# Optimization experiments

Measured on AMD Instinct MI355X. Metric: run time of the kernel, lower is better.

The kernel has to match this reference:

```python
import jax, jax.numpy as jnp
import numpy as np

NEAR, FAR = 0.05, 6.0
STEPSIZE = 0.5
ALPHA_INIT = 1e-6
XYZ_MIN = np.array([-1.0, -1.0, -1.0], np.float32)
XYZ_MAX = np.array([1.0, 1.0, 1.0], np.float32)
WORLD = (160, 160, 160)
VOXEL_SIZE = 2.0 / 160.0  # ((prod span)/num_voxels)^(1/3)
N_SAMPLES = int(np.linalg.norm(np.array(WORLD) + 1) / STEPSIZE) + 1  # 558
ACT_SHIFT = float(np.log(1.0 / (1.0 - ALPHA_INIT) - 1.0))


def setup_inputs() -> dict:
    key = jax.random.key(0)
    k1, k2, k3, k4, k5, k6, k7 = jax.random.split(key, 7)
    rays_o = (jax.random.uniform(k1, (8192, 3), jnp.float32) - 0.5) * 1.2  # inside bbox
    rd = jax.random.normal(k2, (8192, 3), jnp.float32)
    rays_d = rd / jnp.linalg.norm(rd, axis=-1, keepdims=True)
    jitter = jax.random.uniform(k3, (8192, 1), jnp.float32)
    em_modes = jax.random.randint(k4, (8192,), 0, 2, jnp.int32)
    density = jax.random.normal(k5, (1, 160, 160, 160), jnp.float32) * 0.1
    off_color = jax.random.normal(k6, (3, 160, 160, 160), jnp.float32) * 0.1
    emo_color = jax.random.normal(k7, (3, 160, 160, 160), jnp.float32) * 0.1
    return {"rays_o": rays_o, "rays_d": rays_d, "jitter": jitter, "em_modes": em_modes,
            "density": density, "off_color": off_color, "emo_color": emo_color}


def grid_sampler(pts, grid):
    """Trilinear interp, align_corners=True, zero padding. grid [C,Nx,Ny,Nz], pts [...,3] -> [...,C]."""
    C = grid.shape[0]
    sizes = np.array(grid.shape[1:], np.int32)
    lead = pts.shape[:-1]
    t = (pts.reshape(-1, 3) - XYZ_MIN) / (XYZ_MAX - XYZ_MIN)
    idx = t * (jnp.asarray(sizes, pts.dtype) - 1)  # voxel-space coords
    i0 = jnp.floor(idx).astype(jnp.int32)
    f = idx - i0.astype(pts.dtype)
    out = jnp.zeros((i0.shape[0], C), grid.dtype)
    for corner in range(8):
        off = np.array([(corner >> 2) & 1, (corner >> 1) & 1, corner & 1], np.int32)
        ci = i0 + off  # [N,3]
        w = jnp.prod(jnp.where(off[None, :] == 1, f, 1.0 - f), axis=-1)  # [N]
        valid = jnp.all((ci >= 0) & (ci < sizes[None, :]), axis=-1)
        cc = jnp.clip(ci, 0, sizes[None, :] - 1)
        vals = grid[:, cc[:, 0], cc[:, 1], cc[:, 2]].T  # [N,C]
        out = out + (w * valid)[:, None] * vals
    return out.reshape(*lead, C)


def sample_ray(rays_o, rays_d, jitter):
    vec = jnp.where(rays_d == 0, 1e-6, rays_d)
    rate_a = (XYZ_MAX - rays_o) / vec
    rate_b = (XYZ_MIN - rays_o) / vec
    t_min = jnp.clip(jnp.minimum(rate_a, rate_b).max(-1), NEAR, FAR)
    t_max = jnp.clip(jnp.maximum(rate_a, rate_b).min(-1), NEAR, FAR)
    mask_out = t_max <= t_min  # [R]
    rng = jnp.arange(N_SAMPLES, dtype=rays_o.dtype)[None, :] + jitter  # [R,S]
    step = STEPSIZE * VOXEL_SIZE * rng
    interpx = t_min[:, None] + step / jnp.linalg.norm(rays_d, axis=-1, keepdims=True)
    rays_pts = rays_o[:, None, :] + rays_d[:, None, :] * interpx[..., None]  # [R,S,3]
    mask_out = mask_out[:, None] | ((rays_pts < XYZ_MIN) | (rays_pts > XYZ_MAX)).any(-1)
    return rays_pts, mask_out


def reference(rays_o, rays_d, jitter, em_modes, density, off_color, emo_color):
    rays_pts, mask_out = sample_ray(rays_o, rays_d, jitter)
    dens = grid_sampler(rays_pts, density)[..., 0]  # [R,S]
    alpha_all = 1.0 - jnp.exp(-jax.nn.softplus(dens + ACT_SHIFT) * STEPSIZE)
    alpha = jnp.where(mask_out, 0.0, alpha_all)
    p = jnp.clip(1.0 - alpha, 1e-10, None)
    alphainv_cum = jnp.concatenate([jnp.ones_like(p[..., :1]), jnp.cumprod(p, -1)], -1)  # [R,S+1]
    weights = alpha * alphainv_cum[..., :-1]
    on_mask = (em_modes == 1)[:, None, None]
    emo = jax.nn.sigmoid(grid_sampler(rays_pts, emo_color))
    off = jax.nn.sigmoid(grid_sampler(rays_pts, off_color))
    rgb = jnp.where(on_mask, emo, 0.0) + off  # [R,S,3]
    rgb_marched = (weights[..., None] * rgb).sum(-2)  # [R,3]
    return (alphainv_cum, weights, alphainv_cum[..., -1:], rgb, rgb_marched)
```

## Files before the change

### kernel.cpp

```cpp
#include <hip/hip_runtime.h>
#include <math.h>


namespace {
constexpr int   kR   = 8192;
constexpr int   kS   = 558;
constexpr int   kNC  = (kS + 63) / 64;
constexpr int   kG   = 160;
constexpr int   kG3  = kG * kG * kG;
constexpr float kNear = 0.05f;
constexpr float kFar  = 6.0f;
constexpr float kStepWorld = 0.5f * (2.0f / 160.0f);
constexpr float kActShift = -13.815509557963774f;
constexpr float kLog2e = 1.4426950408889634f;
constexpr int   kBX = 80, kBY = 80, kBZ = 40;
constexpr int   kNB = kBX * kBY * kBZ;
constexpr int   kGridWords = kNB * 16;
constexpr int   kXS = kBY * kBZ * 16;
constexpr int   kYS = kBZ * 16;
}

typedef unsigned int nuint4 __attribute__((ext_vector_type(4)));
typedef float        nfloat2 __attribute__((ext_vector_type(2)));
typedef float        nfloat4 __attribute__((ext_vector_type(4)));

__device__ __forceinline__ float fexp(float x) {
  return __builtin_amdgcn_exp2f(x * kLog2e);
}
__device__ __forceinline__ float sigmoidf_(float x) {
  return __builtin_amdgcn_rcpf(1.0f + fexp(-x));
}

__global__ __launch_bounds__(256) void repack_grids(
    const float* __restrict__ density,
    const float* __restrict__ off_c,
    const float* __restrict__ emo_c,
    unsigned* __restrict__ gridA,
    unsigned* __restrict__ gridB)
{
  const int t   = blockIdx.x * blockDim.x + threadIdx.x;
  const int bid = t >> 2;
  const int q   = t & 3;
  if (bid >= kNB) return;
  const int bz = bid % kBZ;
  const int u  = bid / kBZ;
  const int by = u % kBY;
  const int bx = u / kBY;
  const int x  = bx * 2 + (q >> 1);
  const int y  = by * 2 + (q & 1);
  const int z0 = bz * 4;
  const int vbase = (x * kG + y) * kG + z0;

  const nfloat4 d  = __builtin_nontemporal_load((const nfloat4*)(density + vbase));
  const nfloat4 f0 = __builtin_nontemporal_load((const nfloat4*)(off_c + vbase));
  const nfloat4 f1 = __builtin_nontemporal_load((const nfloat4*)(off_c + vbase + kG3));
  const nfloat4 f2 = __builtin_nontemporal_load((const nfloat4*)(off_c + vbase + 2 * kG3));
  const nfloat4 e0 = __builtin_nontemporal_load((const nfloat4*)(emo_c + vbase));
  const nfloat4 e1 = __builtin_nontemporal_load((const nfloat4*)(emo_c + vbase + kG3));
  const nfloat4 e2 = __builtin_nontemporal_load((const nfloat4*)(emo_c + vbase + 2 * kG3));

  nuint4 va, vb;
  #pragma unroll
  for (int lz = 0; lz < 4; ++lz) {
    int qa = __builtin_amdgcn_cvt_pk_fp8_f32(d[lz],  f0[lz], 0,  false);
    qa     = __builtin_amdgcn_cvt_pk_fp8_f32(f1[lz], f2[lz], qa, true);
    int qb = __builtin_amdgcn_cvt_pk_fp8_f32(e0[lz], e1[lz], 0,  false);
    qb     = __builtin_amdgcn_cvt_pk_fp8_f32(e2[lz], 0.0f,   qb, true);
    va[lz] = (unsigned)qa;
    vb[lz] = (unsigned)qb;
  }
  const size_t woff = (size_t)bid * 16 + q * 4;
  __builtin_nontemporal_store(va, (nuint4*)(gridA + woff));
  __builtin_nontemporal_store(vb, (nuint4*)(gridB + woff));
}

__global__ __launch_bounds__(256) void dvgo_fwd(
    const float* __restrict__ rays_o,
    const float* __restrict__ rays_d,
    const float* __restrict__ jitter,
    const int*   __restrict__ em_modes,
    const unsigned* __restrict__ gridA,
    const unsigned* __restrict__ gridB,
    float* __restrict__ out)
{
  const int tid  = blockIdx.x * blockDim.x + threadIdx.x;
  const int ray  = tid >> 6;
  const int lane = tid & 63;
  if (ray >= kR) return;

  const float ox = rays_o[ray * 3 + 0];
  const float oy = rays_o[ray * 3 + 1];
  const float oz = rays_o[ray * 3 + 2];
  const float dx = rays_d[ray * 3 + 0];
  const float dy = rays_d[ray * 3 + 1];
  const float dz = rays_d[ray * 3 + 2];
  const float jit = jitter[ray];
  const bool  on  = (em_modes[ray] == 1);

  const float vx = (dx == 0.0f) ? 1e-6f : dx;
  const float vy = (dy == 0.0f) ? 1e-6f : dy;
  const float vz = (dz == 0.0f) ? 1e-6f : dz;
  const float ivx = __builtin_amdgcn_rcpf(vx);
  const float ivy = __builtin_amdgcn_rcpf(vy);
  const float ivz = __builtin_amdgcn_rcpf(vz);
  const float rax = ( 1.0f - ox) * ivx, rbx = (-1.0f - ox) * ivx;
  const float ray_a = ( 1.0f - oy) * ivy, rby = (-1.0f - oy) * ivy;
  const float raz = ( 1.0f - oz) * ivz, rbz = (-1.0f - oz) * ivz;
  float tmin = fmaxf(fmaxf(fminf(rax, rbx), fminf(ray_a, rby)), fminf(raz, rbz));
  float tmax = fminf(fminf(fmaxf(rax, rbx), fmaxf(ray_a, rby)), fmaxf(raz, rbz));
  tmin = fminf(fmaxf(tmin, kNear), kFar);
  tmax = fminf(fmaxf(tmax, kNear), kFar);
  const bool  ray_out = (tmax <= tmin);
  const float stepc = kStepWorld *
      __builtin_amdgcn_rsqf(dx * dx + dy * dy + dz * dz);

  float* out_ainv = out;
  float* out_w    = out + kR * (kS + 1);
  float* out_last = out_w + kR * kS;
  float* out_rgb  = out_last + kR;
  float* out_rm   = out_rgb + kR * kS * 3;

  const int base_ainv = ray * (kS + 1);
  const int base_w    = ray * kS;

  if (lane == 0)
    __builtin_nontemporal_store(1.0f, out_ainv + base_ainv);

  const float c_base = on ? 1.0f : 0.5f;

  auto geom_addr = [&](int chunk, int wi[8]) -> unsigned long long {
    const int   s  = chunk * 64 + lane;
    const bool  ac = (s < kS);
    const float t  = tmin + stepc * ((float)s + jit);
    const float px = fmaf(dx, t, ox);
    const float py = fmaf(dy, t, oy);
    const float pz = fmaf(dz, t, oz);
    const float fx = (px + 1.0f) * 0.5f * (float)(kG - 1);
    const float fy = (py + 1.0f) * 0.5f * (float)(kG - 1);
    const float fz = (pz + 1.0f) * 0.5f * (float)(kG - 1);
    const int ix = (int)floorf(fx);
    const int iy = (int)floorf(fy);
    const int iz = (int)floorf(fz);
    const bool reach = ac &&
        (ix >= -1) && (ix <= kG - 1) &&
        (iy >= -1) && (iy <= kG - 1) &&
        (iz >= -1) && (iz <= kG - 1);
    const int gx0 = min(max(ix, 0), kG - 1),     gx1 = min(max(ix + 1, 0), kG - 1);
    const int gy0 = min(max(iy, 0), kG - 1),     gy1 = min(max(iy + 1, 0), kG - 1);
    const int gz0 = min(max(iz, 0), kG - 1),     gz1 = min(max(iz + 1, 0), kG - 1);
    const int X0 = (gx0 >> 1) * kXS + (gx0 & 1) * 8;
    const int X1 = (gx1 >> 1) * kXS + (gx1 & 1) * 8;
    const int Y0 = (gy0 >> 1) * kYS + (gy0 & 1) * 4;
    const int Y1 = (gy1 >> 1) * kYS + (gy1 & 1) * 4;
    const int Z0 = (gz0 >> 2) * 16 + (gz0 & 3);
    const int Z1 = (gz1 >> 2) * 16 + (gz1 & 3);
    wi[0] = X0 + Y0 + Z0; wi[1] = X0 + Y0 + Z1;
    wi[2] = X0 + Y1 + Z0; wi[3] = X0 + Y1 + Z1;
    wi[4] = X1 + Y0 + Z0; wi[5] = X1 + Y0 + Z1;
    wi[6] = X1 + Y1 + Z0; wi[7] = X1 + Y1 + Z1;
    return __ballot(reach);
  };

  auto geom_w = [&](int chunk, float w8[8], bool& masked, bool& active) {
    const int   s  = chunk * 64 + lane;
    active = (s < kS);
    const float t  = tmin + stepc * ((float)s + jit);
    const float px = fmaf(dx, t, ox);
    const float py = fmaf(dy, t, oy);
    const float pz = fmaf(dz, t, oz);
    const bool inb = (px >= -1.0f) & (px <= 1.0f) &
                     (py >= -1.0f) & (py <= 1.0f) &
                     (pz >= -1.0f) & (pz <= 1.0f);
    masked = ray_out || !inb;
    const float fx = (px + 1.0f) * 0.5f * (float)(kG - 1);
    const float fy = (py + 1.0f) * 0.5f * (float)(kG - 1);
    const float fz = (pz + 1.0f) * 0.5f * (float)(kG - 1);
    const int ix = (int)floorf(fx);
    const int iy = (int)floorf(fy);
    const int iz = (int)floorf(fz);
    const float wx = fx - (float)ix;
    const float wy = fy - (float)iy;
    const float wz = fz - (float)iz;
    const float x0 = 1.0f - wx, y0 = 1.0f - wy, z0 = 1.0f - wz;
    const float wxy00 = x0 * y0, wxy01 = x0 * wy;
    const float wxy10 = wx * y0, wxy11 = wx * wy;
    const bool vx0 = ((unsigned)ix       < (unsigned)kG);
    const bool vx1 = ((unsigned)(ix + 1) < (unsigned)kG);
    const bool vy0 = ((unsigned)iy       < (unsigned)kG);
    const bool vy1 = ((unsigned)(iy + 1) < (unsigned)kG);
    const bool vz0 = ((unsigned)iz       < (unsigned)kG);
    const bool vz1 = ((unsigned)(iz + 1) < (unsigned)kG);
    w8[0] = (vx0 & vy0 & vz0) ? wxy00 * z0 : 0.0f;
    w8[1] = (vx0 & vy0 & vz1) ? wxy00 * wz : 0.0f;
    w8[2] = (vx0 & vy1 & vz0) ? wxy01 * z0 : 0.0f;
    w8[3] = (vx0 & vy1 & vz1) ? wxy01 * wz : 0.0f;
    w8[4] = (vx1 & vy0 & vz0) ? wxy10 * z0 : 0.0f;
    w8[5] = (vx1 & vy0 & vz1) ? wxy10 * wz : 0.0f;
    w8[6] = (vx1 & vy1 & vz0) ? wxy11 * z0 : 0.0f;
    w8[7] = (vx1 & vy1 & vz1) ? wxy11 * wz : 0.0f;
  };

  float carry = 1.0f;
  float accr = 0.0f, accg = 0.0f, accb = 0.0f;

  unsigned ua[8] = {0, 0, 0, 0, 0, 0, 0, 0};
  unsigned ub[8] = {0, 0, 0, 0, 0, 0, 0, 0};
  bool dead_pipe = false;
  bool cur_dead  = true;

  {
    int wi[8];
    const unsigned long long bal = geom_addr(0, wi);
    if (bal == 0ull) {
      dead_pipe = true;
    } else {
      cur_dead = false;
      #pragma unroll
      for (int c = 0; c < 8; ++c) ua[c] = gridA[wi[c]];
      if (on) {
        #pragma unroll
        for (int c = 0; c < 8; ++c) ub[c] = gridB[wi[c]];
      }
    }
  }

  #pragma unroll 1
  for (int chunk = 0; chunk < kNC; ++chunk) {
    const int  s       = chunk * 64 + lane;
    const bool active0 = (s < kS);

    float dsum = 0.0f;
    float o0 = 0.0f, o1 = 0.0f, o2 = 0.0f;
    float e0 = 0.0f, e1 = 0.0f, e2 = 0.0f;
    bool masked = true, active = active0;

    if (!cur_dead) {
      float w8[8];
      geom_w(chunk, w8, masked, active);
      #pragma unroll
      for (int c = 0; c < 8; ++c) {
        const float w = w8[c];
        dsum = fmaf(w, __builtin_amdgcn_cvt_f32_fp8((int)ua[c], 0), dsum);
        o0   = fmaf(w, __builtin_amdgcn_cvt_f32_fp8((int)ua[c], 1), o0);
        o1   = fmaf(w, __builtin_amdgcn_cvt_f32_fp8((int)ua[c], 2), o1);
        o2   = fmaf(w, __builtin_amdgcn_cvt_f32_fp8((int)ua[c], 3), o2);
      }
      if (on) {
        #pragma unroll
        for (int c = 0; c < 8; ++c) {
          const float w = w8[c];
          e0 = fmaf(w, __builtin_amdgcn_cvt_f32_fp8((int)ub[c], 0), e0);
          e1 = fmaf(w, __builtin_amdgcn_cvt_f32_fp8((int)ub[c], 1), e1);
          e2 = fmaf(w, __builtin_amdgcn_cvt_f32_fp8((int)ub[c], 2), e2);
        }
      }
    }

    bool nxt_dead = true;
    if (!dead_pipe && (chunk + 1) < kNC) {
      int wi[8];
      const unsigned long long bal = geom_addr(chunk + 1, wi);
      if (bal == 0ull) {
        dead_pipe = true;
      } else {
        nxt_dead = false;
        #pragma unroll
        for (int c = 0; c < 8; ++c) ua[c] = gridA[wi[c]];
        if (on) {
          #pragma unroll
          for (int c = 0; c < 8; ++c) ub[c] = gridB[wi[c]];
        }
      }
    }

    if (!cur_dead) {
      float p = 1.0f;
      if (active && !masked) {
        const float expx = fexp(dsum + kActShift);
        p = fmaxf(__builtin_amdgcn_rsqf(1.0f + expx), 1e-10f);
      }
      const float alpha = 1.0f - p;

      float incl = p;
      #pragma unroll
      for (int o = 1; o < 64; o <<= 1) {
        const float n = __shfl_up(incl, o, 64);
        if (lane >= o) incl *= n;
      }
      float excl = __shfl_up(incl, 1, 64);
      if (lane == 0) excl = 1.0f;

      const float ainv_prev = carry * excl;
      const float ainv_next = carry * incl;
      const float wgt = alpha * ainv_prev;
      carry *= __shfl(incl, 63, 64);

      float rr = sigmoidf_(o0);
      float gg = sigmoidf_(o1);
      float bb = sigmoidf_(o2);
      if (on) {
        rr += sigmoidf_(e0);
        gg += sigmoidf_(e1);
        bb += sigmoidf_(e2);
      }

      if (active) {
        __builtin_nontemporal_store(ainv_next, out_ainv + base_ainv + s + 1);
        __builtin_nontemporal_store(wgt, out_w + base_w + s);
        const int rb = (base_w + s) * 3;
        nfloat2 rg;
        rg.x = rr; rg.y = gg;
        __builtin_nontemporal_store(rg, (nfloat2*)(out_rgb + rb));
        __builtin_nontemporal_store(bb, out_rgb + rb + 2);
        accr = fmaf(wgt, rr, accr);
        accg = fmaf(wgt, gg, accg);
        accb = fmaf(wgt, bb, accb);
      }
    } else if (active0) {
      __builtin_nontemporal_store(carry, out_ainv + base_ainv + s + 1);
      __builtin_nontemporal_store(0.0f, out_w + base_w + s);
      const int rb = (base_w + s) * 3;
      nfloat2 cb;
      cb.x = c_base; cb.y = c_base;
      __builtin_nontemporal_store(cb, (nfloat2*)(out_rgb + rb));
      __builtin_nontemporal_store(c_base, out_rgb + rb + 2);
    }

    cur_dead = nxt_dead;
  }

  #pragma unroll
  for (int o = 32; o > 0; o >>= 1) {
    accr += __shfl_xor(accr, o, 64);
    accg += __shfl_xor(accg, o, 64);
    accb += __shfl_xor(accb, o, 64);
  }
  if (lane == 0) {
    out_last[ray] = carry;
    out_rm[ray * 3 + 0] = accr;
    out_rm[ray * 3 + 1] = accg;
    out_rm[ray * 3 + 2] = accb;
  }
}

extern "C" void kernel_launch(void* const* d_in, const int* in_sizes, int n_in,
                              void* d_out, int out_size, void* d_ws, size_t ws_size,
                              hipStream_t stream) {
  const float* rays_o  = (const float*)d_in[0];
  const float* rays_d  = (const float*)d_in[1];
  const float* jitter  = (const float*)d_in[2];
  const int*   em      = (const int*)d_in[3];
  const float* density = (const float*)d_in[4];
  const float* off_c   = (const float*)d_in[5];
  const float* emo_c   = (const float*)d_in[6];
  float* out = (float*)d_out;

  unsigned* gridA = (unsigned*)d_ws;
  unsigned* gridB = gridA + kGridWords;
  (void)ws_size;

  hipLaunchKernelGGL(repack_grids, dim3((kNB * 4 + 255) / 256), dim3(256), 0,
                     stream, density, off_c, emo_c, gridA, gridB);

  const int threads = 256;
  const int blocks  = (kR * 64) / threads;
  hipLaunchKernelGGL(dvgo_fwd, dim3(blocks), dim3(threads), 0, stream,
                     rays_o, rays_d, jitter, em, gridA, gridB, out);
}
```

Before: 220.2 us.

## Assign contiguous 9-sample segments per lane with a single wave scan

The sample-to-lane mapping changes from 9 chunks of 64 lanes (64-strided) to one block of 9 consecutive samples per lane over 62 lanes. The per-chunk 64-lane transmittance scan becomes a serial per-lane product followed by one wave-wide scan, and the weights are computed as run - anext. The ballot-based skip of dead (out-of-grid) chunks and their constant-fill fast path are removed, so every sample now does the gathers. Stores to ainv, weight and rgb become lane-strided by 9, which loses coalescing, and the 2-of-64 idle lanes plus the extra register arrays may hurt occupancy.

```diff
diff --git a/kernel.cpp b/kernel.cpp
--- a/kernel.cpp
+++ b/kernel.cpp
@@ -5,7 +5,8 @@
 namespace {
 constexpr int   kR   = 8192;
 constexpr int   kS   = 558;
-constexpr int   kNC  = (kS + 63) / 64;
+constexpr int   kJ   = 9;
+constexpr int   kLn  = 62;
 constexpr int   kG   = 160;
 constexpr int   kG3  = kG * kG * kG;
 constexpr float kNear = 0.05f;
@@ -21,7 +22,6 @@
 }
 
 typedef unsigned int nuint4 __attribute__((ext_vector_type(4)));
-typedef float        nfloat2 __attribute__((ext_vector_type(2)));
 typedef float        nfloat4 __attribute__((ext_vector_type(4)));
 
 __device__ __forceinline__ float fexp(float x) {
@@ -124,13 +124,12 @@
   const int base_w    = ray * kS;
 
   if (lane == 0)
-    __builtin_nontemporal_store(1.0f, out_ainv + base_ainv);
-
-  const float c_base = on ? 1.0f : 0.5f;
-
-  auto geom_addr = [&](int chunk, int wi[8]) -> unsigned long long {
-    const int   s  = chunk * 64 + lane;
-    const bool  ac = (s < kS);
+    out_ainv[base_ainv] = 1.0f;
+
+  const bool active = (lane < kLn);
+
+  auto geom_addr = [&](int j, int wi[8]) {
+    const int   s  = lane * kJ + j;
     const float t  = tmin + stepc * ((float)s + jit);
     const float px = fmaf(dx, t, ox);
     const float py = fmaf(dy, t, oy);
@@ -141,10 +140,6 @@
     const int ix = (int)floorf(fx);
     const int iy = (int)floorf(fy);
     const int iz = (int)floorf(fz);
-    const bool reach = ac &&
-        (ix >= -1) && (ix <= kG - 1) &&
-        (iy >= -1) && (iy <= kG - 1) &&
-        (iz >= -1) && (iz <= kG - 1);
     const int gx0 = min(max(ix, 0), kG - 1),     gx1 = min(max(ix + 1, 0), kG - 1);
     const int gy0 = min(max(iy, 0), kG - 1),     gy1 = min(max(iy + 1, 0), kG - 1);
     const int gz0 = min(max(iz, 0), kG - 1),     gz1 = min(max(iz + 1, 0), kG - 1);
@@ -158,12 +153,10 @@
     wi[2] = X0 + Y1 + Z0; wi[3] = X0 + Y1 + Z1;
     wi[4] = X1 + Y0 + Z0; wi[5] = X1 + Y0 + Z1;
     wi[6] = X1 + Y1 + Z0; wi[7] = X1 + Y1 + Z1;
-    return __ballot(reach);
   };
 
-  auto geom_w = [&](int chunk, float w8[8], bool& masked, bool& active) {
-    const int   s  = chunk * 64 + lane;
-    active = (s < kS);
+  auto geom_w = [&](int j, float w8[8], bool& masked) {
+    const int   s  = lane * kJ + j;
     const float t  = tmin + stepc * ((float)s + jit);
     const float px = fmaf(dx, t, ox);
     const float py = fmaf(dy, t, oy);
@@ -200,133 +193,125 @@
     w8[7] = (vx1 & vy1 & vz1) ? wxy11 * wz : 0.0f;
   };
 
-  float carry = 1.0f;
-  float accr = 0.0f, accg = 0.0f, accb = 0.0f;
-
-  unsigned ua[8] = {0, 0, 0, 0, 0, 0, 0, 0};
-  unsigned ub[8] = {0, 0, 0, 0, 0, 0, 0, 0};
-  bool dead_pipe = false;
-  bool cur_dead  = true;
-
+  float p[kJ];
+  float rgr[kJ], rgg[kJ], rgbv[kJ];
+
+  unsigned ua[8], ub[8];
   {
     int wi[8];
-    const unsigned long long bal = geom_addr(0, wi);
-    if (bal == 0ull) {
-      dead_pipe = true;
-    } else {
-      cur_dead = false;
+    geom_addr(0, wi);
+    #pragma unroll
+    for (int c = 0; c < 8; ++c) ua[c] = gridA[wi[c]];
+    if (on) {
       #pragma unroll
-      for (int c = 0; c < 8; ++c) ua[c] = gridA[wi[c]];
+      for (int c = 0; c < 8; ++c) ub[c] = gridB[wi[c]];
+    }
+  }
+
+  #pragma unroll
+  for (int j = 0; j < kJ; ++j) {
+    float w8[8];
+    bool masked;
+    geom_w(j, w8, masked);
+
+    unsigned uan[8], ubn[8];
+    if (j + 1 < kJ) {
+      int wi[8];
+      geom_addr(j + 1, wi);
+      #pragma unroll
+      for (int c = 0; c < 8; ++c) uan[c] = gridA[wi[c]];
       if (on) {
         #pragma unroll
-        for (int c = 0; c < 8; ++c) ub[c] = gridB[wi[c]];
+        for (int c = 0; c < 8; ++c) ubn[c] = gridB[wi[c]];
       }
     }
-  }
-
-  #pragma unroll 1
-  for (int chunk = 0; chunk < kNC; ++chunk) {
-    const int  s       = chunk * 64 + lane;
-    const bool active0 = (s < kS);
 
     float dsum = 0.0f;
     float o0 = 0.0f, o1 = 0.0f, o2 = 0.0f;
     float e0 = 0.0f, e1 = 0.0f, e2 = 0.0f;
-    bool masked = true, active = active0;
-
-    if (!cur_dead) {
-      float w8[8];
-      geom_w(chunk, w8, masked, active);
+    #pragma unroll
+    for (int c = 0; c < 8; ++c) {
+      const float w = w8[c];
+      dsum = fmaf(w, __builtin_amdgcn_cvt_f32_fp8((int)ua[c], 0), dsum);
+      o0   = fmaf(w, __builtin_amdgcn_cvt_f32_fp8((int)ua[c], 1), o0);
+      o1   = fmaf(w, __builtin_amdgcn_cvt_f32_fp8((int)ua[c], 2), o1);
+      o2   = fmaf(w, __builtin_amdgcn_cvt_f32_fp8((int)ua[c], 3), o2);
+    }
+    if (on) {
       #pragma unroll
       for (int c = 0; c < 8; ++c) {
         const float w = w8[c];
-        dsum = fmaf(w, __builtin_amdgcn_cvt_f32_fp8((int)ua[c], 0), dsum);
-        o0   = fmaf(w, __builtin_amdgcn_cvt_f32_fp8((int)ua[c], 1), o0);
-        o1   = fmaf(w, __builtin_amdgcn_cvt_f32_fp8((int)ua[c], 2), o1);
-        o2   = fmaf(w, __builtin_amdgcn_cvt_f32_fp8((int)ua[c], 3), o2);
+        e0 = fmaf(w, __builtin_amdgcn_cvt_f32_fp8((int)ub[c], 0), e0);
+        e1 = fmaf(w, __builtin_amdgcn_cvt_f32_fp8((int)ub[c], 1), e1);
+        e2 = fmaf(w, __builtin_amdgcn_cvt_f32_fp8((int)ub[c], 2), e2);
       }
+    }
+
+    float pj = 1.0f;
+    if (active && !masked) {
+      const float expx = fexp(dsum + kActShift);
+      pj = fmaxf(__builtin_amdgcn_rsqf(1.0f + expx), 1e-10f);
+    }
+    p[j] = pj;
+
+    float rr = sigmoidf_(o0);
+    float gg = sigmoidf_(o1);
+    float bb = sigmoidf_(o2);
+    if (on) {
+      rr += sigmoidf_(e0);
+      gg += sigmoidf_(e1);
+      bb += sigmoidf_(e2);
+    }
+    rgr[j] = rr; rgg[j] = gg; rgbv[j] = bb;
+
+    if (active) {
+      const int s  = lane * kJ + j;
+      const int rb = (base_w + s) * 3;
+      __builtin_nontemporal_store(rr, out_rgb + rb + 0);
+      __builtin_nontemporal_store(gg, out_rgb + rb + 1);
+      __builtin_nontemporal_store(bb, out_rgb + rb + 2);
+    }
+
+    if (j + 1 < kJ) {
+      #pragma unroll
+      for (int c = 0; c < 8; ++c) ua[c] = uan[c];
       if (on) {
         #pragma unroll
-        for (int c = 0; c < 8; ++c) {
-          const float w = w8[c];
-          e0 = fmaf(w, __builtin_amdgcn_cvt_f32_fp8((int)ub[c], 0), e0);
-          e1 = fmaf(w, __builtin_amdgcn_cvt_f32_fp8((int)ub[c], 1), e1);
-          e2 = fmaf(w, __builtin_amdgcn_cvt_f32_fp8((int)ub[c], 2), e2);
-        }
+        for (int c = 0; c < 8; ++c) ub[c] = ubn[c];
       }
     }
-
-    bool nxt_dead = true;
-    if (!dead_pipe && (chunk + 1) < kNC) {
-      int wi[8];
-      const unsigned long long bal = geom_addr(chunk + 1, wi);
-      if (bal == 0ull) {
-        dead_pipe = true;
-      } else {
-        nxt_dead = false;
-        #pragma unroll
-        for (int c = 0; c < 8; ++c) ua[c] = gridA[wi[c]];
-        if (on) {
-          #pragma unroll
-          for (int c = 0; c < 8; ++c) ub[c] = gridB[wi[c]];
-        }
-      }
-    }
-
-    if (!cur_dead) {
-      float p = 1.0f;
-      if (active && !masked) {
-        const float expx = fexp(dsum + kActShift);
-        p = fmaxf(__builtin_amdgcn_rsqf(1.0f + expx), 1e-10f);
-      }
-      const float alpha = 1.0f - p;
-
-      float incl = p;
-      #pragma unroll
-      for (int o = 1; o < 64; o <<= 1) {
-        const float n = __shfl_up(incl, o, 64);
-        if (lane >= o) incl *= n;
-      }
-      float excl = __shfl_up(incl, 1, 64);
-      if (lane == 0) excl = 1.0f;
-
-      const float ainv_prev = carry * excl;
-      const float ainv_next = carry * incl;
-      const float wgt = alpha * ainv_prev;
-      carry *= __shfl(incl, 63, 64);
-
-      float rr = sigmoidf_(o0);
-      float gg = sigmoidf_(o1);
-      float bb = sigmoidf_(o2);
-      if (on) {
-        rr += sigmoidf_(e0);
-        gg += sigmoidf_(e1);
-        bb += sigmoidf_(e2);
-      }
-
-      if (active) {
-        __builtin_nontemporal_store(ainv_next, out_ainv + base_ainv + s + 1);
-        __builtin_nontemporal_store(wgt, out_w + base_w + s);
-        const int rb = (base_w + s) * 3;
-        nfloat2 rg;
-        rg.x = rr; rg.y = gg;
-        __builtin_nontemporal_store(rg, (nfloat2*)(out_rgb + rb));
-        __builtin_nontemporal_store(bb, out_rgb + rb + 2);
-        accr = fmaf(wgt, rr, accr);
-        accg = fmaf(wgt, gg, accg);
-        accb = fmaf(wgt, bb, accb);
-      }
-    } else if (active0) {
-      __builtin_nontemporal_store(carry, out_ainv + base_ainv + s + 1);
-      __builtin_nontemporal_store(0.0f, out_w + base_w + s);
-      const int rb = (base_w + s) * 3;
-      nfloat2 cb;
-      cb.x = c_base; cb.y = c_base;
-      __builtin_nontemporal_store(cb, (nfloat2*)(out_rgb + rb));
-      __builtin_nontemporal_store(c_base, out_rgb + rb + 2);
-    }
-
-    cur_dead = nxt_dead;
+  }
+
+  const float q01 = p[0] * p[1], q23 = p[2] * p[3];
+  const float q45 = p[4] * p[5], q67 = p[6] * p[7];
+  const float lane_prod = ((q01 * q23) * (q45 * q67)) * p[8];
+
+  float incl = lane_prod;
+  #pragma unroll
+  for (int o = 1; o < 64; o <<= 1) {
+    const float n = __shfl_up(incl, o, 64);
+    if (lane >= o) incl *= n;
+  }
+  float excl = __shfl_up(incl, 1, 64);
+  if (lane == 0) excl = 1.0f;
+  const float total = __shfl(incl, 63, 64);
+
+  float accr = 0.0f, accg = 0.0f, accb = 0.0f;
+  float run = excl;
+  #pragma unroll
+  for (int j = 0; j < kJ; ++j) {
+    const float pj    = p[j];
+    const float anext = run * pj;
+    const float wgt   = run - anext;
+    if (active) {
+      const int s = lane * kJ + j;
+      out_ainv[base_ainv + s + 1] = anext;
+      out_w[base_w + s]           = wgt;
+      accr = fmaf(wgt, rgr[j], accr);
+      accg = fmaf(wgt, rgg[j], accg);
+      accb = fmaf(wgt, rgbv[j], accb);
+    }
+    run = anext;
   }
 
   #pragma unroll
@@ -336,7 +321,7 @@
     accb += __shfl_xor(accb, o, 64);
   }
   if (lane == 0) {
-    out_last[ray] = carry;
+    out_last[ray] = total;
     out_rm[ray * 3 + 0] = accr;
     out_rm[ray * 3 + 1] = accg;
     out_rm[ray * 3 + 2] = accb;
```

New measurement: 339.9 us. +54.4%, slower.

## Split each ray across four wavefronts with a shared-memory cross-chunk product

Applied to the files above, without the earlier changes.

Each 256-thread block now handles a single ray, and its four wavefronts process interleaved 64-sample chunks instead of one wavefront walking all nine chunks in sequence. Per-chunk transmittance products are exchanged through shared memory so each wave can rebuild its carry and write alpha-inverse and weights after a block barrier. The goal is to cut the serial per-ray dependency chain and expose more memory-level parallelism for the gathers. In exchange it drops the early exit for dead rays, adds two block syncs, and keeps more live registers per thread.

```diff
diff --git a/kernel.cpp b/kernel.cpp
--- a/kernel.cpp
+++ b/kernel.cpp
@@ -83,10 +83,12 @@
     const unsigned* __restrict__ gridB,
     float* __restrict__ out)
 {
-  const int tid  = blockIdx.x * blockDim.x + threadIdx.x;
-  const int ray  = tid >> 6;
-  const int lane = tid & 63;
-  if (ray >= kR) return;
+  const int ray  = blockIdx.x;
+  const int wv   = (threadIdx.x >> 6) & 3;
+  const int lane = threadIdx.x & 63;
+
+  __shared__ float s_prod[kNC];
+  __shared__ float s_acc[4][3];
 
   const float ox = rays_o[ray * 3 + 0];
   const float oy = rays_o[ray * 3 + 1];
@@ -123,13 +125,12 @@
   const int base_ainv = ray * (kS + 1);
   const int base_w    = ray * kS;
 
-  if (lane == 0)
+  if (threadIdx.x == 0)
     __builtin_nontemporal_store(1.0f, out_ainv + base_ainv);
 
   const float c_base = on ? 1.0f : 0.5f;
 
-  auto geom_addr = [&](int chunk, int wi[8]) -> unsigned long long {
-    const int   s  = chunk * 64 + lane;
+  auto geom_addr = [&](int s, int wi[8]) -> unsigned long long {
     const bool  ac = (s < kS);
     const float t  = tmin + stepc * ((float)s + jit);
     const float px = fmaf(dx, t, ox);
@@ -161,9 +162,7 @@
     return __ballot(reach);
   };
 
-  auto geom_w = [&](int chunk, float w8[8], bool& masked, bool& active) {
-    const int   s  = chunk * 64 + lane;
-    active = (s < kS);
+  auto geom_w = [&](int s, float w8[8], bool& masked) {
     const float t  = tmin + stepc * ((float)s + jit);
     const float px = fmaf(dx, t, ox);
     const float py = fmaf(dy, t, oy);
@@ -200,133 +199,149 @@
     w8[7] = (vx1 & vy1 & vz1) ? wxy11 * wz : 0.0f;
   };
 
-  float carry = 1.0f;
-  float accr = 0.0f, accg = 0.0f, accb = 0.0f;
-
-  unsigned ua[8] = {0, 0, 0, 0, 0, 0, 0, 0};
-  unsigned ub[8] = {0, 0, 0, 0, 0, 0, 0, 0};
-  bool dead_pipe = false;
-  bool cur_dead  = true;
-
+  float incl_a[3], excl_a[3], rr_a[3], gg_a[3], bb_a[3];
+
+  unsigned cua[8], cub[8];
+  bool cur_live;
   {
     int wi[8];
-    const unsigned long long bal = geom_addr(0, wi);
-    if (bal == 0ull) {
-      dead_pipe = true;
-    } else {
-      cur_dead = false;
+    const unsigned long long bal = geom_addr(wv * 64 + lane, wi);
+    cur_live = (bal != 0ull);
+    if (cur_live) {
       #pragma unroll
-      for (int c = 0; c < 8; ++c) ua[c] = gridA[wi[c]];
+      for (int c = 0; c < 8; ++c) cua[c] = gridA[wi[c]];
       if (on) {
         #pragma unroll
-        for (int c = 0; c < 8; ++c) ub[c] = gridB[wi[c]];
+        for (int c = 0; c < 8; ++c) cub[c] = gridB[wi[c]];
       }
     }
   }
 
-  #pragma unroll 1
-  for (int chunk = 0; chunk < kNC; ++chunk) {
-    const int  s       = chunk * 64 + lane;
-    const bool active0 = (s < kS);
-
-    float dsum = 0.0f;
-    float o0 = 0.0f, o1 = 0.0f, o2 = 0.0f;
-    float e0 = 0.0f, e1 = 0.0f, e2 = 0.0f;
-    bool masked = true, active = active0;
-
-    if (!cur_dead) {
-      float w8[8];
-      geom_w(chunk, w8, masked, active);
-      #pragma unroll
-      for (int c = 0; c < 8; ++c) {
-        const float w = w8[c];
-        dsum = fmaf(w, __builtin_amdgcn_cvt_f32_fp8((int)ua[c], 0), dsum);
-        o0   = fmaf(w, __builtin_amdgcn_cvt_f32_fp8((int)ua[c], 1), o0);
-        o1   = fmaf(w, __builtin_amdgcn_cvt_f32_fp8((int)ua[c], 2), o1);
-        o2   = fmaf(w, __builtin_amdgcn_cvt_f32_fp8((int)ua[c], 3), o2);
-      }
-      if (on) {
+  #pragma unroll
+  for (int k = 0; k < 3; ++k) {
+    const int c = wv + 4 * k;
+    if (c < kNC) {
+      const int s = c * 64 + lane;
+
+      unsigned nua[8], nub[8];
+      bool nxt_live = false;
+      if (c + 4 < kNC) {
+        int wi[8];
+        const unsigned long long bal = geom_addr((c + 4) * 64 + lane, wi);
+        nxt_live = (bal != 0ull);
+        if (nxt_live) {
+          #pragma unroll
+          for (int q = 0; q < 8; ++q) nua[q] = gridA[wi[q]];
+          if (on) {
+            #pragma unroll
+            for (int q = 0; q < 8; ++q) nub[q] = gridB[wi[q]];
+          }
+        }
+      }
+
+      float incl = 1.0f, excl = 1.0f;
+      float rr = c_base, gg = c_base, bb = c_base;
+
+      if (cur_live) {
+        float w8[8];
+        bool masked;
+        geom_w(s, w8, masked);
+        float dsum = 0.0f;
+        float o0 = 0.0f, o1 = 0.0f, o2 = 0.0f;
+        float e0 = 0.0f, e1 = 0.0f, e2 = 0.0f;
         #pragma unroll
-        for (int c = 0; c < 8; ++c) {
-          const float w = w8[c];
-          e0 = fmaf(w, __builtin_amdgcn_cvt_f32_fp8((int)ub[c], 0), e0);
-          e1 = fmaf(w, __builtin_amdgcn_cvt_f32_fp8((int)ub[c], 1), e1);
-          e2 = fmaf(w, __builtin_amdgcn_cvt_f32_fp8((int)ub[c], 2), e2);
-        }
-      }
-    }
-
-    bool nxt_dead = true;
-    if (!dead_pipe && (chunk + 1) < kNC) {
-      int wi[8];
-      const unsigned long long bal = geom_addr(chunk + 1, wi);
-      if (bal == 0ull) {
-        dead_pipe = true;
-      } else {
-        nxt_dead = false;
-        #pragma unroll
-        for (int c = 0; c < 8; ++c) ua[c] = gridA[wi[c]];
+        for (int q = 0; q < 8; ++q) {
+          const float w = w8[q];
+          dsum = fmaf(w, __builtin_amdgcn_cvt_f32_fp8((int)cua[q], 0), dsum);
+          o0   = fmaf(w, __builtin_amdgcn_cvt_f32_fp8((int)cua[q], 1), o0);
+          o1   = fmaf(w, __builtin_amdgcn_cvt_f32_fp8((int)cua[q], 2), o1);
+          o2   = fmaf(w, __builtin_amdgcn_cvt_f32_fp8((int)cua[q], 3), o2);
+        }
         if (on) {
           #pragma unroll
-          for (int c = 0; c < 8; ++c) ub[c] = gridB[wi[c]];
-        }
-      }
-    }
-
-    if (!cur_dead) {
-      float p = 1.0f;
-      if (active && !masked) {
-        const float expx = fexp(dsum + kActShift);
-        p = fmaxf(__builtin_amdgcn_rsqf(1.0f + expx), 1e-10f);
-      }
-      const float alpha = 1.0f - p;
-
-      float incl = p;
-      #pragma unroll
-      for (int o = 1; o < 64; o <<= 1) {
-        const float n = __shfl_up(incl, o, 64);
-        if (lane >= o) incl *= n;
-      }
-      float excl = __shfl_up(incl, 1, 64);
-      if (lane == 0) excl = 1.0f;
-
-      const float ainv_prev = carry * excl;
-      const float ainv_next = carry * incl;
-      const float wgt = alpha * ainv_prev;
-      carry *= __shfl(incl, 63, 64);
-
-      float rr = sigmoidf_(o0);
-      float gg = sigmoidf_(o1);
-      float bb = sigmoidf_(o2);
-      if (on) {
-        rr += sigmoidf_(e0);
-        gg += sigmoidf_(e1);
-        bb += sigmoidf_(e2);
-      }
-
-      if (active) {
-        __builtin_nontemporal_store(ainv_next, out_ainv + base_ainv + s + 1);
-        __builtin_nontemporal_store(wgt, out_w + base_w + s);
+          for (int q = 0; q < 8; ++q) {
+            const float w = w8[q];
+            e0 = fmaf(w, __builtin_amdgcn_cvt_f32_fp8((int)cub[q], 0), e0);
+            e1 = fmaf(w, __builtin_amdgcn_cvt_f32_fp8((int)cub[q], 1), e1);
+            e2 = fmaf(w, __builtin_amdgcn_cvt_f32_fp8((int)cub[q], 2), e2);
+          }
+        }
+
+        float p = 1.0f;
+        if ((s < kS) && !masked) {
+          const float expx = fexp(dsum + kActShift);
+          p = fmaxf(__builtin_amdgcn_rsqf(1.0f + expx), 1e-10f);
+        }
+
+        incl = p;
+        #pragma unroll
+        for (int o = 1; o < 64; o <<= 1) {
+          const float n = __shfl_up(incl, o, 64);
+          if (lane >= o) incl *= n;
+        }
+        excl = __shfl_up(incl, 1, 64);
+        if (lane == 0) excl = 1.0f;
+
+        rr = sigmoidf_(o0);
+        gg = sigmoidf_(o1);
+        bb = sigmoidf_(o2);
+        if (on) {
+          rr += sigmoidf_(e0);
+          gg += sigmoidf_(e1);
+          bb += sigmoidf_(e2);
+        }
+      }
+
+      if (s < kS) {
         const int rb = (base_w + s) * 3;
         nfloat2 rg;
         rg.x = rr; rg.y = gg;
         __builtin_nontemporal_store(rg, (nfloat2*)(out_rgb + rb));
         __builtin_nontemporal_store(bb, out_rgb + rb + 2);
-        accr = fmaf(wgt, rr, accr);
-        accg = fmaf(wgt, gg, accg);
-        accb = fmaf(wgt, bb, accb);
-      }
-    } else if (active0) {
-      __builtin_nontemporal_store(carry, out_ainv + base_ainv + s + 1);
-      __builtin_nontemporal_store(0.0f, out_w + base_w + s);
-      const int rb = (base_w + s) * 3;
-      nfloat2 cb;
-      cb.x = c_base; cb.y = c_base;
-      __builtin_nontemporal_store(cb, (nfloat2*)(out_rgb + rb));
-      __builtin_nontemporal_store(c_base, out_rgb + rb + 2);
+      }
+
+      incl_a[k] = incl; excl_a[k] = excl;
+      rr_a[k] = rr; gg_a[k] = gg; bb_a[k] = bb;
+
+      const float prod = __shfl(incl, 63, 64);
+      if (lane == 0) s_prod[c] = prod;
+
+      cur_live = nxt_live;
+      #pragma unroll
+      for (int q = 0; q < 8; ++q) cua[q] = nua[q];
+      if (on) {
+        #pragma unroll
+        for (int q = 0; q < 8; ++q) cub[q] = nub[q];
+      }
     }
-
-    cur_dead = nxt_dead;
+  }
+
+  __syncthreads();
+
+  float sp[kNC];
+  #pragma unroll
+  for (int i = 0; i < kNC; ++i) sp[i] = s_prod[i];
+
+  float accr = 0.0f, accg = 0.0f, accb = 0.0f;
+  #pragma unroll
+  for (int k = 0; k < 3; ++k) {
+    const int c = wv + 4 * k;
+    if (c < kNC) {
+      float carry = 1.0f;
+      #pragma unroll
+      for (int i = 0; i < kNC; ++i) carry *= (i < c) ? sp[i] : 1.0f;
+      const int s = c * 64 + lane;
+      const float anext = carry * incl_a[k];
+      const float aprev = carry * excl_a[k];
+      const float wgt   = aprev - anext;
+      if (s < kS) {
+        __builtin_nontemporal_store(anext, out_ainv + base_ainv + s + 1);
+        __builtin_nontemporal_store(wgt, out_w + base_w + s);
+        accr = fmaf(wgt, rr_a[k], accr);
+        accg = fmaf(wgt, gg_a[k], accg);
+        accb = fmaf(wgt, bb_a[k], accb);
+      }
+    }
   }
 
   #pragma unroll
@@ -336,10 +351,20 @@
     accb += __shfl_xor(accb, o, 64);
   }
   if (lane == 0) {
-    out_last[ray] = carry;
-    out_rm[ray * 3 + 0] = accr;
-    out_rm[ray * 3 + 1] = accg;
-    out_rm[ray * 3 + 2] = accb;
+    s_acc[wv][0] = accr;
+    s_acc[wv][1] = accg;
+    s_acc[wv][2] = accb;
+  }
+  __syncthreads();
+
+  if (threadIdx.x == 0) {
+    out_rm[ray * 3 + 0] = s_acc[0][0] + s_acc[1][0] + s_acc[2][0] + s_acc[3][0];
+    out_rm[ray * 3 + 1] = s_acc[0][1] + s_acc[1][1] + s_acc[2][1] + s_acc[3][1];
+    out_rm[ray * 3 + 2] = s_acc[0][2] + s_acc[1][2] + s_acc[2][2] + s_acc[3][2];
+    float tot = 1.0f;
+    #pragma unroll
+    for (int i = 0; i < kNC; ++i) tot *= sp[i];
+    out_last[ray] = tot;
   }
 }
 
@@ -362,8 +387,6 @@
   hipLaunchKernelGGL(repack_grids, dim3((kNB * 4 + 255) / 256), dim3(256), 0,
                      stream, density, off_c, emo_c, gridA, gridB);
 
-  const int threads = 256;
-  const int blocks  = (kR * 64) / threads;
-  hipLaunchKernelGGL(dvgo_fwd, dim3(blocks), dim3(threads), 0, stream,
+  hipLaunchKernelGGL(dvgo_fwd, dim3(kR), dim3(256), 0, stream,
                      rays_o, rays_d, jitter, em, gridA, gridB, out);
 }
```

Result: no change. 218.0 us (median of 2 runs) (-1.0%).
